# Optimization experiments

Hardware: AMD Instinct MI355X
Metric: run time of the kernel (lower is better)

The kernel has to match this reference:

```python
import jax, jax.numpy as jnp
from jax import lax
import numpy as np

B, T, H, IN = 256, 1024, 256, 1

def setup_inputs() -> dict:
    key = jax.random.key(0)
    ks = jax.random.split(key, 9)
    s = 1.0 / np.sqrt(H)  # PyTorch default uniform(-1/sqrt(H), 1/sqrt(H)); use scaled normal
    return {
        "x": jax.random.normal(ks[0], (B, T, IN), jnp.float32),
        "W_ih0": jax.random.normal(ks[1], (4 * H, IN), jnp.float32) * s,
        "W_hh0": jax.random.normal(ks[2], (4 * H, H), jnp.float32) * s,
        "b_ih0": jax.random.normal(ks[3], (4 * H,), jnp.float32) * s,
        "b_hh0": jax.random.normal(ks[4], (4 * H,), jnp.float32) * s,
        "W_ih1": jax.random.normal(ks[5], (4 * H, H), jnp.float32) * s,
        "W_hh1": jax.random.normal(ks[6], (4 * H, H), jnp.float32) * s,
        "b_ih1": jax.random.normal(ks[7], (4 * H,), jnp.float32) * s,
        "b_hh1": jax.random.normal(ks[8], (4 * H,), jnp.float32) * s,
    }

def _lstm_layer(x, W_ih, W_hh, b_ih, b_hh):
    # x: [B, T, D_in] -> (y [B, T, H], h_T [B, H], c_T [B, H]); gates ordered i,f,g,o (PyTorch)
    b, t = x.shape[0], x.shape[1]
    h = W_hh.shape[1]
    # precompute input projection for all timesteps: [T, B, 4H]
    xp = jnp.swapaxes(jnp.einsum('btd,gd->btg', x, W_ih) + b_ih + b_hh, 0, 1)

    def step(carry, xt):
        hprev, cprev = carry
        gates = xt + hprev @ W_hh.T  # [B, 4H]
        i, f, g, o = jnp.split(gates, 4, axis=-1)
        i = jax.nn.sigmoid(i)
        f = jax.nn.sigmoid(f)
        g = jnp.tanh(g)
        o = jax.nn.sigmoid(o)
        c = f * cprev + i * g
        hnew = o * jnp.tanh(c)
        return (hnew, c), hnew

    h0 = jnp.zeros((b, h), x.dtype)
    (hT, cT), ys = lax.scan(step, (h0, h0), xp)
    return jnp.swapaxes(ys, 0, 1), hT, cT

def reference(x, W_ih0, W_hh0, b_ih0, b_hh0, W_ih1, W_hh1, b_ih1, b_hh1):
    y0, h0, c0 = _lstm_layer(x, W_ih0, W_hh0, b_ih0, b_hh0)
    # inter-layer dropout(0.1) is train-only; inference = identity
    _, h1, c1 = _lstm_layer(y0, W_ih1, W_hh1, b_ih1, b_hh1)
    h_n = jnp.stack([h0, h1], axis=0)  # [num_layers, B, H]
    c_n = jnp.stack([c0, c1], axis=0)
    return h_n, c_n
```

## Files before the change

kernel.cpp:

```cpp
#include <hip/hip_runtime.h>


#define TSTEPS 1024u
#define FMAGIC 0x5A5A0000u

typedef __attribute__((ext_vector_type(8))) short bf16x8;
typedef __attribute__((ext_vector_type(4))) float f32x4;

__device__ __forceinline__ unsigned short f2bf(float f) {
  unsigned u = __float_as_uint(f);
  u += 0x7FFFu + ((u >> 16) & 1u);
  return (unsigned short)(u >> 16);
}
__device__ __forceinline__ float sigm(float x) { return 1.0f / (1.0f + __expf(-x)); }
__device__ __forceinline__ float tanh_f(float x) {
  float xc = fminf(fmaxf(x, -15.0f), 15.0f);
  float e = __expf(2.0f * xc);
  return (e - 1.0f) / (e + 1.0f);
}

__global__ __launch_bounds__(256, 1) void lstm2_v7(
    const float* __restrict__ x,
    const float* __restrict__ Wih0,
    const float* __restrict__ Whh0,
    const float* __restrict__ bih0, const float* __restrict__ bhh0,
    const float* __restrict__ Wih1,
    const float* __restrict__ Whh1,
    const float* __restrict__ bih1, const float* __restrict__ bhh1,
    float* __restrict__ out,
    unsigned long long* __restrict__ fastb,
    unsigned long long* __restrict__ slowb,
    unsigned* __restrict__ ctrl,
    unsigned* __restrict__ flagF,
    unsigned* __restrict__ flagS)
{
  const int bid  = blockIdx.x;
  const int c    = bid & 15;
  const int iw   = bid >> 4;
  const int tid  = threadIdx.x;
  const int lane = tid & 63;
  const int wv   = tid >> 6;
  const int hi   = lane >> 4;
  const int lm   = lane & 15;

  unsigned myxcc;
  asm volatile("s_getreg_b32 %0, hwreg(HW_REG_XCC_ID)" : "=s"(myxcc));
  myxcc &= 0xFu;
  if (tid == 0)
    __hip_atomic_store(&ctrl[bid], FMAGIC | myxcc,
                       __ATOMIC_RELAXED, __HIP_MEMORY_SCOPE_AGENT);

  bf16x8 w0[8], wi1[8], wh1[8];
  {
    const int wrow = (lm & 3) * 256 + (iw << 4) + (wv << 2) + (lm >> 2);
    const int kb   = hi << 3;
#pragma unroll
    for (int kk = 0; kk < 8; ++kk) {
      const int k0 = kk * 32 + kb;
      const float* p0 = Whh0 + (size_t)wrow * 256 + k0;
      const float* p1 = Wih1 + (size_t)wrow * 256 + k0;
      const float* p2 = Whh1 + (size_t)wrow * 256 + k0;
      bf16x8 a, b, cc;
#pragma unroll
      for (int e = 0; e < 8; ++e) {
        a[e]  = (short)f2bf(p0[e]);
        b[e]  = (short)f2bf(p1[e]);
        cc[e] = (short)f2bf(p2[e]);
      }
      w0[kk] = a; wi1[kk] = b; wh1[kk] = cc;
    }
  }

  const int rowE = lm;
  const int jg   = (iw << 4) + (wv << 2) + hi;
  float wx[4], bs0[4], bs1[4];
#pragma unroll
  for (int r = 0; r < 4; ++r) {
    const int col = (r << 8) + jg;
    wx[r]  = Wih0[col];
    bs0[r] = bih0[col] + bhh0[col];
    bs1[r] = bih1[col] + bhh1[col];
  }

  unsigned ofs_[8], lofs_[8];
#pragma unroll
  for (int i = 0; i < 8; ++i) {
    const int n   = tid + 256 * i;
    const int L   = n >> 10;
    const int row = (n >> 6) & 15;
    const int q   = n & 63;
    ofs_[i]  = (unsigned)(((c * 2 + L) * 16 + row) * 64 + q);
    lofs_[i] = (unsigned)(L * 4224 + row * 264 + q * 4);
  }

  __shared__ unsigned s_uni;
  if (tid == 0) {
    if (iw == 0) {
      unsigned x0 = 0, uni = 1u;
      for (int k = 0; k < 16 && uni; ++k) {
        unsigned v; int g2 = 0;
        for (;;) {
          v = __hip_atomic_load(&ctrl[c + 16 * k], __ATOMIC_RELAXED, __HIP_MEMORY_SCOPE_AGENT);
          if ((v & 0xFFFF0000u) == FMAGIC) break;
          if (++g2 > (1 << 15)) { uni = 0u; break; }
        }
        if (uni) {
          const unsigned xc = v & 0xFFFFu;
          if (k == 0) x0 = xc; else if (xc != x0) uni = 0u;
        }
      }
      __hip_atomic_store(&ctrl[256 + c], FMAGIC | uni,
                         __ATOMIC_RELAXED, __HIP_MEMORY_SCOPE_AGENT);
    }
    unsigned uni = 0u; int g2 = 0;
    for (;;) {
      unsigned v = __hip_atomic_load(&ctrl[256 + c], __ATOMIC_RELAXED, __HIP_MEMORY_SCOPE_AGENT);
      if ((v & 0xFFFF0000u) == FMAGIC) { uni = v & 1u; break; }
      if (++g2 > (1 << 15)) break;
    }
    s_uni = uni;
  }
  __syncthreads();
  const bool uniform = (s_uni != 0u);
  unsigned long long* pollD = uniform ? fastb : slowb;
  unsigned*           pollF = uniform ? flagF : flagS;
  unsigned*           myFlagF = &flagF[(c << 6) + (iw << 2) + wv];
  unsigned*           myFlagS = &flagS[(c << 6) + (iw << 2) + wv];
  unsigned*           fl      = pollF + (c << 6);

  __shared__ __align__(16) unsigned short A[2 * 2 * 16 * 264];

  const float* xrow = x + (size_t)((c << 4) + rowE) * TSTEPS;
  float4 xq = {0.f, 0.f, 0.f, 0.f};

  float c0 = 0.f, h0f = 0.f, c1 = 0.f, h1f = 0.f;
  bool dead = false;

  for (unsigned s = 0; s <= TSTEPS; ++s) {
    if ((s & 3u) == 0u && s < TSTEPS) xq = *(const float4*)(xrow + s);
    const float xv = (s & 2u) ? ((s & 1u) ? xq.w : xq.z) : ((s & 1u) ? xq.y : xq.x);

    unsigned long long* fb = fastb + (size_t)((s + 1u) & 1u) * 32768u;
    unsigned long long* sb = slowb + (size_t)((s + 1u) & 1u) * 32768u;
    const unsigned long long* pb = pollD + (size_t)(s & 1u) * 32768u;
    unsigned short* Ap = A + (s & 1u) * 8448u;

    if (s == 0) {
      for (int z = tid; z < 8448; z += 256) ((unsigned*)A)[z] = 0u;
    } else {
      const unsigned want = FMAGIC + s;
      int guard = 0;
      while (!dead) {
        const unsigned f = __hip_atomic_load(fl + lane, __ATOMIC_RELAXED, __HIP_MEMORY_SCOPE_AGENT);
        if (__all((int)((f - want) < 0x10000u))) break;
        if (++guard > (1 << 12)) dead = true;
      }
      unsigned long long vv[8];
#pragma unroll
      for (int i = 0; i < 8; ++i)
        vv[i] = __hip_atomic_load(pb + ofs_[i], __ATOMIC_RELAXED, __HIP_MEMORY_SCOPE_AGENT);
#pragma unroll
      for (int i = 0; i < 8; ++i)
        *(unsigned long long*)&Ap[lofs_[i]] = vv[i];
    }
    __syncthreads();

    bf16x8 af0[8];
    f32x4 acc0a = {0.f, 0.f, 0.f, 0.f}, acc0b = {0.f, 0.f, 0.f, 0.f};
    const unsigned short* a0p = Ap + lm * 264 + (hi << 3);
    const unsigned short* a1p = a0p + 4224;
#pragma unroll
    for (int kk = 0; kk < 4; ++kk) {
      af0[kk] = *(const bf16x8*)(a0p + kk * 32);
      acc0a = __builtin_amdgcn_mfma_f32_16x16x32_bf16(w0[kk], af0[kk], acc0a, 0, 0, 0);
    }
#pragma unroll
    for (int kk = 4; kk < 8; ++kk) {
      af0[kk] = *(const bf16x8*)(a0p + kk * 32);
      acc0b = __builtin_amdgcn_mfma_f32_16x16x32_bf16(w0[kk], af0[kk], acc0b, 0, 0, 0);
    }

    f32x4 a1a0 = {0.f, 0.f, 0.f, 0.f}, a1a1 = {0.f, 0.f, 0.f, 0.f};
    f32x4 a1b0 = {0.f, 0.f, 0.f, 0.f}, a1b1 = {0.f, 0.f, 0.f, 0.f};
#pragma unroll
    for (int kk = 0; kk < 4; ++kk) {
      a1a0 = __builtin_amdgcn_mfma_f32_16x16x32_bf16(wi1[kk], af0[kk], a1a0, 0, 0, 0);
      const bf16x8 a1f = *(const bf16x8*)(a1p + kk * 32);
      a1b0 = __builtin_amdgcn_mfma_f32_16x16x32_bf16(wh1[kk], a1f, a1b0, 0, 0, 0);
    }
#pragma unroll
    for (int kk = 4; kk < 8; ++kk) {
      a1a1 = __builtin_amdgcn_mfma_f32_16x16x32_bf16(wi1[kk], af0[kk], a1a1, 0, 0, 0);
      const bf16x8 a1f = *(const bf16x8*)(a1p + kk * 32);
      a1b1 = __builtin_amdgcn_mfma_f32_16x16x32_bf16(wh1[kk], a1f, a1b1, 0, 0, 0);
    }

    if (s < TSTEPS) {
      const float pi = (acc0a[0] + acc0b[0]) + xv * wx[0] + bs0[0];
      const float pf = (acc0a[1] + acc0b[1]) + xv * wx[1] + bs0[1];
      const float pg = (acc0a[2] + acc0b[2]) + xv * wx[2] + bs0[2];
      const float po = (acc0a[3] + acc0b[3]) + xv * wx[3] + bs0[3];
      const float ig = sigm(pi), fg = sigm(pf), gv = tanh_f(pg), og = sigm(po);
      c0  = fg * c0 + ig * gv;
      h0f = og * tanh_f(c0);

      const int v   = (int)(unsigned)f2bf(h0f);
      const int p16 = __shfl_xor(v, 16);
      const unsigned part = (unsigned)(unsigned short)v | ((unsigned)(unsigned short)p16 << 16);
      const unsigned p32  = (unsigned)__shfl_xor((int)part, 32);
      const unsigned long long v64 = (unsigned long long)part | ((unsigned long long)p32 << 32);
      const unsigned i0 = ((c * 2 + 0) * 16 + (unsigned)rowE) * 64 + (unsigned)((iw << 2) + wv);
      if (hi == 0) {
        __hip_atomic_store(fb + i0, v64, __ATOMIC_RELAXED, __HIP_MEMORY_SCOPE_WORKGROUP);
        if (!uniform)
          __hip_atomic_store(sb + i0, v64, __ATOMIC_RELAXED, __HIP_MEMORY_SCOPE_AGENT);
      }
    }

    if (s >= 1u) {
      const float pi = (a1a0[0] + a1a1[0]) + (a1b0[0] + a1b1[0]) + bs1[0];
      const float pf = (a1a0[1] + a1a1[1]) + (a1b0[1] + a1b1[1]) + bs1[1];
      const float pg = (a1a0[2] + a1a1[2]) + (a1b0[2] + a1b1[2]) + bs1[2];
      const float po = (a1a0[3] + a1a1[3]) + (a1b0[3] + a1b1[3]) + bs1[3];
      const float ig = sigm(pi), fg = sigm(pf), gv = tanh_f(pg), og = sigm(po);
      c1  = fg * c1 + ig * gv;
      h1f = og * tanh_f(c1);
    }
    if (s < TSTEPS) {
      const int v   = (int)(unsigned)f2bf(h1f);
      const int p16 = __shfl_xor(v, 16);
      const unsigned part = (unsigned)(unsigned short)v | ((unsigned)(unsigned short)p16 << 16);
      const unsigned p32  = (unsigned)__shfl_xor((int)part, 32);
      const unsigned long long v64 = (unsigned long long)part | ((unsigned long long)p32 << 32);
      const unsigned i1 = ((c * 2 + 1) * 16 + (unsigned)rowE) * 64 + (unsigned)((iw << 2) + wv);
      if (hi == 0) {
        __hip_atomic_store(fb + i1, v64, __ATOMIC_RELAXED, __HIP_MEMORY_SCOPE_WORKGROUP);
        if (!uniform)
          __hip_atomic_store(sb + i1, v64, __ATOMIC_RELAXED, __HIP_MEMORY_SCOPE_AGENT);
      }

      asm volatile("s_waitcnt vmcnt(0)" ::: "memory");
      if (lane == 0) {
        const unsigned fv = FMAGIC + s + 1u;
        if (uniform)
          __hip_atomic_store(myFlagF, fv, __ATOMIC_RELAXED, __HIP_MEMORY_SCOPE_WORKGROUP);
        else
          __hip_atomic_store(myFlagS, fv, __ATOMIC_RELAXED, __HIP_MEMORY_SCOPE_AGENT);
      }
    }
  }

  {
    const int b  = (c << 4) + rowE;
    const size_t o = (size_t)b * 256 + jg;
    out[o]                  = h0f;
    out[65536 + o]          = h1f;
    out[131072 + o]         = c0;
    out[131072 + 65536 + o] = c1;
  }
}

extern "C" void kernel_launch(void* const* d_in, const int* in_sizes, int n_in,
                              void* d_out, int out_size, void* d_ws, size_t ws_size,
                              hipStream_t stream) {
  const float* x    = (const float*)d_in[0];
  const float* Wih0 = (const float*)d_in[1];
  const float* Whh0 = (const float*)d_in[2];
  const float* bih0 = (const float*)d_in[3];
  const float* bhh0 = (const float*)d_in[4];
  const float* Wih1 = (const float*)d_in[5];
  const float* Whh1 = (const float*)d_in[6];
  const float* bih1 = (const float*)d_in[7];
  const float* bhh1 = (const float*)d_in[8];

  unsigned long long* fastb = (unsigned long long*)d_ws;
  unsigned long long* slowb;
  unsigned *ctrl, *flagF, *flagS;
  if (ws_size >= (1u << 20) + 12288u) {
    slowb = fastb + 65536;
    ctrl  = (unsigned*)(fastb + 131072);
    flagF = ctrl + 512;
    flagS = flagF + 1024;
  } else {
    slowb = fastb;
    ctrl  = (unsigned*)((char*)d_ws + (512u << 10));
    flagF = ctrl + 512;
    flagS = flagF;
  }

  lstm2_v7<<<256, 256, 0, stream>>>(x, Wih0, Whh0, bih0, bhh0,
                                    Wih1, Whh1, bih1, bhh1,
                                    (float*)d_out, fastb, slowb, ctrl, flagF, flagS);
}
```

Measured before the change: 1.807 ms.

## Split LSTM layers into separate producer/consumer blocks pipelined across timesteps

Launches twice as many blocks: one set runs layer 0 and another runs layer 1, synchronised through per-step global flags. Layer-0 blocks read their recurrent h fragments straight from global memory with no LDS staging, and they raise their wave priority. This shortens the per-step critical path of layer 0 and lets layer 1 trail it in a pipelined fashion. The cost is double the block count (launch bounds raised to 2 per CU), extra flag polling across both layers, and a write-after-read hazard on the double-buffered exchange that the extra flag checks have to cover.

```diff
diff --git a/kernel.cpp b/kernel.cpp
--- a/kernel.cpp
+++ b/kernel.cpp
@@ -19,7 +19,9 @@
   return (e - 1.0f) / (e + 1.0f);
 }
 
-__global__ __launch_bounds__(256, 1) void lstm2_v7(
+union FragU { unsigned long long q[2]; bf16x8 v; };
+
+__global__ __launch_bounds__(256, 2) void lstm2_v8(
     const float* __restrict__ x,
     const float* __restrict__ Wih0,
     const float* __restrict__ Whh0,
@@ -35,8 +37,9 @@
     unsigned* __restrict__ flagS)
 {
   const int bid  = blockIdx.x;
+  const int type = bid >> 8;
   const int c    = bid & 15;
-  const int iw   = bid >> 4;
+  const int iw   = (bid >> 4) & 15;
   const int tid  = threadIdx.x;
   const int lane = tid & 63;
   const int wv   = tid >> 6;
@@ -50,57 +53,54 @@
     __hip_atomic_store(&ctrl[bid], FMAGIC | myxcc,
                        __ATOMIC_RELAXED, __HIP_MEMORY_SCOPE_AGENT);
 
-  bf16x8 w0[8], wi1[8], wh1[8];
+  bf16x8 wA[8], wB[8];
   {
     const int wrow = (lm & 3) * 256 + (iw << 4) + (wv << 2) + (lm >> 2);
     const int kb   = hi << 3;
-#pragma unroll
-    for (int kk = 0; kk < 8; ++kk) {
-      const int k0 = kk * 32 + kb;
-      const float* p0 = Whh0 + (size_t)wrow * 256 + k0;
-      const float* p1 = Wih1 + (size_t)wrow * 256 + k0;
-      const float* p2 = Whh1 + (size_t)wrow * 256 + k0;
-      bf16x8 a, b, cc;
-#pragma unroll
-      for (int e = 0; e < 8; ++e) {
-        a[e]  = (short)f2bf(p0[e]);
-        b[e]  = (short)f2bf(p1[e]);
-        cc[e] = (short)f2bf(p2[e]);
-      }
-      w0[kk] = a; wi1[kk] = b; wh1[kk] = cc;
+    if (type == 0) {
+      const float* pA = Whh0 + (size_t)wrow * 256 + kb;
+#pragma unroll
+      for (int kk = 0; kk < 8; ++kk) {
+        bf16x8 a;
+#pragma unroll
+        for (int e = 0; e < 8; ++e) a[e] = (short)f2bf(pA[kk * 32 + e]);
+        wA[kk] = a;
+      }
+    } else {
+      const float* pA = Wih1 + (size_t)wrow * 256 + kb;
+      const float* pB = Whh1 + (size_t)wrow * 256 + kb;
+#pragma unroll
+      for (int kk = 0; kk < 8; ++kk) {
+        bf16x8 a, b;
+#pragma unroll
+        for (int e = 0; e < 8; ++e) {
+          a[e] = (short)f2bf(pA[kk * 32 + e]);
+          b[e] = (short)f2bf(pB[kk * 32 + e]);
+        }
+        wA[kk] = a; wB[kk] = b;
+      }
     }
   }
 
   const int rowE = lm;
   const int jg   = (iw << 4) + (wv << 2) + hi;
-  float wx[4], bs0[4], bs1[4];
+  float wx[4], bs[4];
 #pragma unroll
   for (int r = 0; r < 4; ++r) {
     const int col = (r << 8) + jg;
-    wx[r]  = Wih0[col];
-    bs0[r] = bih0[col] + bhh0[col];
-    bs1[r] = bih1[col] + bhh1[col];
-  }
-
-  unsigned ofs_[8], lofs_[8];
-#pragma unroll
-  for (int i = 0; i < 8; ++i) {
-    const int n   = tid + 256 * i;
-    const int L   = n >> 10;
-    const int row = (n >> 6) & 15;
-    const int q   = n & 63;
-    ofs_[i]  = (unsigned)(((c * 2 + L) * 16 + row) * 64 + q);
-    lofs_[i] = (unsigned)(L * 4224 + row * 264 + q * 4);
+    if (type == 0) { wx[r] = Wih0[col]; bs[r] = bih0[col] + bhh0[col]; }
+    else           { wx[r] = 0.f;       bs[r] = bih1[col] + bhh1[col]; }
   }
 
   __shared__ unsigned s_uni;
   if (tid == 0) {
-    if (iw == 0) {
+    if (type == 0 && iw == 0) {
       unsigned x0 = 0, uni = 1u;
-      for (int k = 0; k < 16 && uni; ++k) {
+      for (int k = 0; k < 32 && uni; ++k) {
+        const int b2 = (k < 16) ? (c + 16 * k) : (256 + c + 16 * (k - 16));
         unsigned v; int g2 = 0;
         for (;;) {
-          v = __hip_atomic_load(&ctrl[c + 16 * k], __ATOMIC_RELAXED, __HIP_MEMORY_SCOPE_AGENT);
+          v = __hip_atomic_load(&ctrl[b2], __ATOMIC_RELAXED, __HIP_MEMORY_SCOPE_AGENT);
           if ((v & 0xFFFF0000u) == FMAGIC) break;
           if (++g2 > (1 << 15)) { uni = 0u; break; }
         }
@@ -109,12 +109,12 @@
           if (k == 0) x0 = xc; else if (xc != x0) uni = 0u;
         }
       }
-      __hip_atomic_store(&ctrl[256 + c], FMAGIC | uni,
+      __hip_atomic_store(&ctrl[512 + c], FMAGIC | uni,
                          __ATOMIC_RELAXED, __HIP_MEMORY_SCOPE_AGENT);
     }
     unsigned uni = 0u; int g2 = 0;
     for (;;) {
-      unsigned v = __hip_atomic_load(&ctrl[256 + c], __ATOMIC_RELAXED, __HIP_MEMORY_SCOPE_AGENT);
+      unsigned v = __hip_atomic_load(&ctrl[512 + c], __ATOMIC_RELAXED, __HIP_MEMORY_SCOPE_AGENT);
       if ((v & 0xFFFF0000u) == FMAGIC) { uni = v & 1u; break; }
       if (++g2 > (1 << 15)) break;
     }
@@ -124,82 +124,64 @@
   const bool uniform = (s_uni != 0u);
   unsigned long long* pollD = uniform ? fastb : slowb;
   unsigned*           pollF = uniform ? flagF : flagS;
-  unsigned*           myFlagF = &flagF[(c << 6) + (iw << 2) + wv];
-  unsigned*           myFlagS = &flagS[(c << 6) + (iw << 2) + wv];
-  unsigned*           fl      = pollF + (c << 6);
-
-  __shared__ __align__(16) unsigned short A[2 * 2 * 16 * 264];
-
-  const float* xrow = x + (size_t)((c << 4) + rowE) * TSTEPS;
-  float4 xq = {0.f, 0.f, 0.f, 0.f};
-
-  float c0 = 0.f, h0f = 0.f, c1 = 0.f, h1f = 0.f;
+  unsigned*           flc   = pollF + c * 128;
+
+  const size_t oBase = (size_t)((c << 4) + rowE) * 256 + jg;
   bool dead = false;
 
-  for (unsigned s = 0; s <= TSTEPS; ++s) {
-    if ((s & 3u) == 0u && s < TSTEPS) xq = *(const float4*)(xrow + s);
-    const float xv = (s & 2u) ? ((s & 1u) ? xq.w : xq.z) : ((s & 1u) ? xq.y : xq.x);
-
-    unsigned long long* fb = fastb + (size_t)((s + 1u) & 1u) * 32768u;
-    unsigned long long* sb = slowb + (size_t)((s + 1u) & 1u) * 32768u;
-    const unsigned long long* pb = pollD + (size_t)(s & 1u) * 32768u;
-    unsigned short* Ap = A + (s & 1u) * 8448u;
-
-    if (s == 0) {
-      for (int z = tid; z < 8448; z += 256) ((unsigned*)A)[z] = 0u;
-    } else {
-      const unsigned want = FMAGIC + s;
-      int guard = 0;
-      while (!dead) {
-        const unsigned f = __hip_atomic_load(fl + lane, __ATOMIC_RELAXED, __HIP_MEMORY_SCOPE_AGENT);
-        if (__all((int)((f - want) < 0x10000u))) break;
-        if (++guard > (1 << 12)) dead = true;
-      }
-      unsigned long long vv[8];
-#pragma unroll
-      for (int i = 0; i < 8; ++i)
-        vv[i] = __hip_atomic_load(pb + ofs_[i], __ATOMIC_RELAXED, __HIP_MEMORY_SCOPE_AGENT);
-#pragma unroll
-      for (int i = 0; i < 8; ++i)
-        *(unsigned long long*)&Ap[lofs_[i]] = vv[i];
-    }
-    __syncthreads();
-
-    bf16x8 af0[8];
-    f32x4 acc0a = {0.f, 0.f, 0.f, 0.f}, acc0b = {0.f, 0.f, 0.f, 0.f};
-    const unsigned short* a0p = Ap + lm * 264 + (hi << 3);
-    const unsigned short* a1p = a0p + 4224;
-#pragma unroll
-    for (int kk = 0; kk < 4; ++kk) {
-      af0[kk] = *(const bf16x8*)(a0p + kk * 32);
-      acc0a = __builtin_amdgcn_mfma_f32_16x16x32_bf16(w0[kk], af0[kk], acc0a, 0, 0, 0);
-    }
-#pragma unroll
-    for (int kk = 4; kk < 8; ++kk) {
-      af0[kk] = *(const bf16x8*)(a0p + kk * 32);
-      acc0b = __builtin_amdgcn_mfma_f32_16x16x32_bf16(w0[kk], af0[kk], acc0b, 0, 0, 0);
-    }
-
-    f32x4 a1a0 = {0.f, 0.f, 0.f, 0.f}, a1a1 = {0.f, 0.f, 0.f, 0.f};
-    f32x4 a1b0 = {0.f, 0.f, 0.f, 0.f}, a1b1 = {0.f, 0.f, 0.f, 0.f};
-#pragma unroll
-    for (int kk = 0; kk < 4; ++kk) {
-      a1a0 = __builtin_amdgcn_mfma_f32_16x16x32_bf16(wi1[kk], af0[kk], a1a0, 0, 0, 0);
-      const bf16x8 a1f = *(const bf16x8*)(a1p + kk * 32);
-      a1b0 = __builtin_amdgcn_mfma_f32_16x16x32_bf16(wh1[kk], a1f, a1b0, 0, 0, 0);
-    }
-#pragma unroll
-    for (int kk = 4; kk < 8; ++kk) {
-      a1a1 = __builtin_amdgcn_mfma_f32_16x16x32_bf16(wi1[kk], af0[kk], a1a1, 0, 0, 0);
-      const bf16x8 a1f = *(const bf16x8*)(a1p + kk * 32);
-      a1b1 = __builtin_amdgcn_mfma_f32_16x16x32_bf16(wh1[kk], a1f, a1b1, 0, 0, 0);
-    }
-
-    if (s < TSTEPS) {
-      const float pi = (acc0a[0] + acc0b[0]) + xv * wx[0] + bs0[0];
-      const float pf = (acc0a[1] + acc0b[1]) + xv * wx[1] + bs0[1];
-      const float pg = (acc0a[2] + acc0b[2]) + xv * wx[2] + bs0[2];
-      const float po = (acc0a[3] + acc0b[3]) + xv * wx[3] + bs0[3];
+  if (type == 0) {
+    __builtin_amdgcn_s_setprio(1);
+    unsigned* myF = &flagF[c * 128 + (iw << 2) + wv];
+    unsigned* myS = &flagS[c * 128 + (iw << 2) + wv];
+    const float* xrow = x + (size_t)((c << 4) + rowE) * TSTEPS;
+    float4 xq = {0.f, 0.f, 0.f, 0.f};
+    float c0 = 0.f, h0f = 0.f;
+
+    for (unsigned s = 0; s < TSTEPS; ++s) {
+      if ((s & 3u) == 0u) xq = *(const float4*)(xrow + s);
+      const float xv = (s & 2u) ? ((s & 1u) ? xq.w : xq.z) : ((s & 1u) ? xq.y : xq.x);
+
+      bf16x8 af0[8];
+      if (s == 0) {
+        const bf16x8 z = {0, 0, 0, 0, 0, 0, 0, 0};
+#pragma unroll
+        for (int kk = 0; kk < 8; ++kk) af0[kk] = z;
+      } else {
+        const unsigned want0 = FMAGIC + s;
+        const unsigned want1 = FMAGIC + s - 1u;
+        const bool chk1 = (s >= 2u);
+        int guard = 0;
+        while (!dead) {
+          const unsigned f0 = __hip_atomic_load(flc + lane, __ATOMIC_RELAXED, __HIP_MEMORY_SCOPE_AGENT);
+          const unsigned f1 = chk1 ? __hip_atomic_load(flc + 64 + lane, __ATOMIC_RELAXED, __HIP_MEMORY_SCOPE_AGENT)
+                                   : want1;
+          const bool ok = ((f0 - want0) < 0x10000u) & ((f1 - want1) < 0x10000u);
+          if (__all(ok)) break;
+          if (++guard > (1 << 13)) dead = true;
+        }
+        const unsigned long long* hb =
+            pollD + (size_t)(s & 1u) * 32768u + (c << 11) + (lm << 6) + (hi << 1);
+#pragma unroll
+        for (int kk = 0; kk < 8; ++kk) {
+          FragU u;
+          u.q[0] = __hip_atomic_load(hb + kk * 8,     __ATOMIC_RELAXED, __HIP_MEMORY_SCOPE_AGENT);
+          u.q[1] = __hip_atomic_load(hb + kk * 8 + 1, __ATOMIC_RELAXED, __HIP_MEMORY_SCOPE_AGENT);
+          af0[kk] = u.v;
+        }
+      }
+
+      f32x4 aca = {0.f, 0.f, 0.f, 0.f}, acb = {0.f, 0.f, 0.f, 0.f};
+#pragma unroll
+      for (int kk = 0; kk < 4; ++kk)
+        aca = __builtin_amdgcn_mfma_f32_16x16x32_bf16(wA[kk], af0[kk], aca, 0, 0, 0);
+#pragma unroll
+      for (int kk = 4; kk < 8; ++kk)
+        acb = __builtin_amdgcn_mfma_f32_16x16x32_bf16(wA[kk], af0[kk], acb, 0, 0, 0);
+
+      const float pi = (aca[0] + acb[0]) + xv * wx[0] + bs[0];
+      const float pf = (aca[1] + acb[1]) + xv * wx[1] + bs[1];
+      const float pg = (aca[2] + acb[2]) + xv * wx[2] + bs[2];
+      const float po = (aca[3] + acb[3]) + xv * wx[3] + bs[3];
       const float ig = sigm(pi), fg = sigm(pf), gv = tanh_f(pg), og = sigm(po);
       c0  = fg * c0 + ig * gv;
       h0f = og * tanh_f(c0);
@@ -210,53 +192,133 @@
       const unsigned p32  = (unsigned)__shfl_xor((int)part, 32);
       const unsigned long long v64 = (unsigned long long)part | ((unsigned long long)p32 << 32);
       const unsigned i0 = ((c * 2 + 0) * 16 + (unsigned)rowE) * 64 + (unsigned)((iw << 2) + wv);
+      unsigned long long* fb = fastb + (size_t)((s + 1u) & 1u) * 32768u;
+      unsigned long long* sb = slowb + (size_t)((s + 1u) & 1u) * 32768u;
       if (hi == 0) {
         __hip_atomic_store(fb + i0, v64, __ATOMIC_RELAXED, __HIP_MEMORY_SCOPE_WORKGROUP);
         if (!uniform)
           __hip_atomic_store(sb + i0, v64, __ATOMIC_RELAXED, __HIP_MEMORY_SCOPE_AGENT);
       }
-    }
-
-    if (s >= 1u) {
-      const float pi = (a1a0[0] + a1a1[0]) + (a1b0[0] + a1b1[0]) + bs1[0];
-      const float pf = (a1a0[1] + a1a1[1]) + (a1b0[1] + a1b1[1]) + bs1[1];
-      const float pg = (a1a0[2] + a1a1[2]) + (a1b0[2] + a1b1[2]) + bs1[2];
-      const float po = (a1a0[3] + a1a1[3]) + (a1b0[3] + a1b1[3]) + bs1[3];
+      asm volatile("s_waitcnt vmcnt(0)" ::: "memory");
+      if (lane == 0) {
+        const unsigned fv = FMAGIC + s + 1u;
+        if (uniform)
+          __hip_atomic_store(myF, fv, __ATOMIC_RELAXED, __HIP_MEMORY_SCOPE_WORKGROUP);
+        else
+          __hip_atomic_store(myS, fv, __ATOMIC_RELAXED, __HIP_MEMORY_SCOPE_AGENT);
+      }
+    }
+    out[oBase]          = h0f;
+    out[131072 + oBase] = c0;
+
+  } else {
+    unsigned* myF = &flagF[c * 128 + 64 + (iw << 2) + wv];
+    unsigned* myS = &flagS[c * 128 + 64 + (iw << 2) + wv];
+
+    unsigned ofs_[8], lofs_[8];
+#pragma unroll
+    for (int i = 0; i < 8; ++i) {
+      const int n   = tid + 256 * i;
+      const int L   = n >> 10;
+      const int row = (n >> 6) & 15;
+      const int q   = n & 63;
+      ofs_[i]  = (unsigned)(((c * 2 + L) * 16 + row) * 64 + q);
+      lofs_[i] = (unsigned)(L * 4224 + row * 264 + q * 4);
+    }
+
+    __shared__ __align__(16) unsigned short A[2 * 2 * 16 * 264];
+    for (int z = tid; z < 8448; z += 256) ((unsigned*)A)[z] = 0u;
+    __syncthreads();
+
+    float c1 = 0.f, h1f = 0.f;
+
+    for (unsigned t = 0; t < TSTEPS; ++t) {
+      {
+        const unsigned want0 = FMAGIC + t + 1u;
+        const unsigned want1 = FMAGIC + t;
+        const bool chk1 = (t >= 1u);
+        int guard = 0;
+        while (!dead) {
+          const unsigned f0 = __hip_atomic_load(flc + lane, __ATOMIC_RELAXED, __HIP_MEMORY_SCOPE_AGENT);
+          const unsigned f1 = chk1 ? __hip_atomic_load(flc + 64 + lane, __ATOMIC_RELAXED, __HIP_MEMORY_SCOPE_AGENT)
+                                   : want1;
+          const bool ok = ((f0 - want0) < 0x10000u) & ((f1 - want1) < 0x10000u);
+          if (__all(ok)) break;
+          if (++guard > (1 << 13)) { dead = true; break; }
+          __builtin_amdgcn_s_sleep(1);
+        }
+      }
+      const unsigned long long* pb0 = pollD + (size_t)((t + 1u) & 1u) * 32768u;
+      const unsigned long long* pb1 = pollD + (size_t)(t & 1u) * 32768u;
+      unsigned short* Ap = A + (t & 1u) * 8448u;
+      {
+        unsigned long long vv[8];
+#pragma unroll
+        for (int i = 0; i < 4; ++i)
+          vv[i] = __hip_atomic_load(pb0 + ofs_[i], __ATOMIC_RELAXED, __HIP_MEMORY_SCOPE_AGENT);
+        if (t >= 1u) {
+#pragma unroll
+          for (int i = 4; i < 8; ++i)
+            vv[i] = __hip_atomic_load(pb1 + ofs_[i], __ATOMIC_RELAXED, __HIP_MEMORY_SCOPE_AGENT);
+        }
+#pragma unroll
+        for (int i = 0; i < 4; ++i)
+          *(unsigned long long*)&Ap[lofs_[i]] = vv[i];
+        if (t >= 1u) {
+#pragma unroll
+          for (int i = 4; i < 8; ++i)
+            *(unsigned long long*)&Ap[lofs_[i]] = vv[i];
+        }
+      }
+      __syncthreads();
+
+      const unsigned short* a0p = Ap + lm * 264 + (hi << 3);
+      const unsigned short* a1p = a0p + 4224;
+      f32x4 p0 = {0.f,0.f,0.f,0.f}, p1 = {0.f,0.f,0.f,0.f};
+      f32x4 q0 = {0.f,0.f,0.f,0.f}, q1 = {0.f,0.f,0.f,0.f};
+#pragma unroll
+      for (int kk = 0; kk < 4; ++kk) {
+        p0 = __builtin_amdgcn_mfma_f32_16x16x32_bf16(wA[kk], *(const bf16x8*)(a0p + kk * 32), p0, 0, 0, 0);
+        q0 = __builtin_amdgcn_mfma_f32_16x16x32_bf16(wB[kk], *(const bf16x8*)(a1p + kk * 32), q0, 0, 0, 0);
+      }
+#pragma unroll
+      for (int kk = 4; kk < 8; ++kk) {
+        p1 = __builtin_amdgcn_mfma_f32_16x16x32_bf16(wA[kk], *(const bf16x8*)(a0p + kk * 32), p1, 0, 0, 0);
+        q1 = __builtin_amdgcn_mfma_f32_16x16x32_bf16(wB[kk], *(const bf16x8*)(a1p + kk * 32), q1, 0, 0, 0);
+      }
+
+      const float pi = (p0[0] + p1[0]) + (q0[0] + q1[0]) + bs[0];
+      const float pf = (p0[1] + p1[1]) + (q0[1] + q1[1]) + bs[1];
+      const float pg = (p0[2] + p1[2]) + (q0[2] + q1[2]) + bs[2];
+      const float po = (p0[3] + p1[3]) + (q0[3] + q1[3]) + bs[3];
       const float ig = sigm(pi), fg = sigm(pf), gv = tanh_f(pg), og = sigm(po);
       c1  = fg * c1 + ig * gv;
       h1f = og * tanh_f(c1);
-    }
-    if (s < TSTEPS) {
+
       const int v   = (int)(unsigned)f2bf(h1f);
       const int p16 = __shfl_xor(v, 16);
       const unsigned part = (unsigned)(unsigned short)v | ((unsigned)(unsigned short)p16 << 16);
       const unsigned p32  = (unsigned)__shfl_xor((int)part, 32);
       const unsigned long long v64 = (unsigned long long)part | ((unsigned long long)p32 << 32);
       const unsigned i1 = ((c * 2 + 1) * 16 + (unsigned)rowE) * 64 + (unsigned)((iw << 2) + wv);
+      unsigned long long* fb = fastb + (size_t)((t + 1u) & 1u) * 32768u;
+      unsigned long long* sb = slowb + (size_t)((t + 1u) & 1u) * 32768u;
       if (hi == 0) {
         __hip_atomic_store(fb + i1, v64, __ATOMIC_RELAXED, __HIP_MEMORY_SCOPE_WORKGROUP);
         if (!uniform)
           __hip_atomic_store(sb + i1, v64, __ATOMIC_RELAXED, __HIP_MEMORY_SCOPE_AGENT);
       }
-
       asm volatile("s_waitcnt vmcnt(0)" ::: "memory");
       if (lane == 0) {
-        const unsigned fv = FMAGIC + s + 1u;
+        const unsigned fv = FMAGIC + t + 1u;
         if (uniform)
-          __hip_atomic_store(myFlagF, fv, __ATOMIC_RELAXED, __HIP_MEMORY_SCOPE_WORKGROUP);
+          __hip_atomic_store(myF, fv, __ATOMIC_RELAXED, __HIP_MEMORY_SCOPE_WORKGROUP);
         else
-          __hip_atomic_store(myFlagS, fv, __ATOMIC_RELAXED, __HIP_MEMORY_SCOPE_AGENT);
-      }
-    }
-  }
-
-  {
-    const int b  = (c << 4) + rowE;
-    const size_t o = (size_t)b * 256 + jg;
-    out[o]                  = h0f;
-    out[65536 + o]          = h1f;
-    out[131072 + o]         = c0;
-    out[131072 + 65536 + o] = c1;
+          __hip_atomic_store(myS, fv, __ATOMIC_RELAXED, __HIP_MEMORY_SCOPE_AGENT);
+      }
+    }
+    out[65536 + oBase]          = h1f;
+    out[131072 + 65536 + oBase] = c1;
   }
 }
 
@@ -276,19 +338,19 @@
   unsigned long long* fastb = (unsigned long long*)d_ws;
   unsigned long long* slowb;
   unsigned *ctrl, *flagF, *flagS;
-  if (ws_size >= (1u << 20) + 12288u) {
+  if (ws_size >= (1u << 20) + 24576u) {
     slowb = fastb + 65536;
     ctrl  = (unsigned*)(fastb + 131072);
-    flagF = ctrl + 512;
-    flagS = flagF + 1024;
+    flagF = ctrl + 2048;
+    flagS = flagF + 2048;
   } else {
     slowb = fastb;
     ctrl  = (unsigned*)((char*)d_ws + (512u << 10));
-    flagF = ctrl + 512;
+    flagF = ctrl + 2048;
     flagS = flagF;
   }
 
-  lstm2_v7<<<256, 256, 0, stream>>>(x, Wih0, Whh0, bih0, bhh0,
+  lstm2_v8<<<512, 256, 0, stream>>>(x, Wih0, Whh0, bih0, bhh0,
                                     Wih1, Whh1, bih1, bhh1,
                                     (float*)d_out, fastb, slowb, ctrl, flagF, flagS);
 }
```

After: 3.335 ms. 1.85x slower.

## Split per-layer flags, stage x in LDS, and publish layer-0 state earlier

Applied to the files above, without the earlier changes.

Layer-0 hidden state is now computed and published, with its own flag, right after its MFMA chain and before the layer-1 MFMAs run. Other blocks can therefore start their next step sooner instead of waiting for both layers. The input sequence x is preloaded into padded shared memory, replacing per-step global float4 loads. Stores are narrowed to 32-bit with a different packing, and the layer-0 MFMA chain is split across four accumulators to shorten the dependency chain. In exchange, pollers must check twice as many flags, and the extra flag write and vmcnt wait per step add overhead.

```diff
diff --git a/kernel.cpp b/kernel.cpp
--- a/kernel.cpp
+++ b/kernel.cpp
@@ -19,7 +19,7 @@
   return (e - 1.0f) / (e + 1.0f);
 }
 
-__global__ __launch_bounds__(256, 1) void lstm2_v7(
+__global__ __launch_bounds__(256, 1) void lstm2_v9(
     const float* __restrict__ x,
     const float* __restrict__ Wih0,
     const float* __restrict__ Whh0,
@@ -71,8 +71,7 @@
     }
   }
 
-  const int rowE = lm;
-  const int jg   = (iw << 4) + (wv << 2) + hi;
+  const int jg = (iw << 4) + (wv << 2) + hi;
   float wx[4], bs0[4], bs1[4];
 #pragma unroll
   for (int r = 0; r < 4; ++r) {
@@ -80,6 +79,15 @@
     wx[r]  = Wih0[col];
     bs0[r] = bih0[col] + bhh0[col];
     bs1[r] = bih1[col] + bhh1[col];
+  }
+
+  __shared__ __align__(16) unsigned short A[2 * 2 * 16 * 264];
+  __shared__ float XL[16 * 1041];
+
+  {
+    const float* xsrc = x + (size_t)(c << 4) * TSTEPS;
+    for (int idx = tid; idx < 16 * 1024; idx += 256)
+      XL[(idx >> 10) * 1041 + (idx & 1023)] = xsrc[idx];
   }
 
   unsigned ofs_[8], lofs_[8];
@@ -124,26 +132,20 @@
   const bool uniform = (s_uni != 0u);
   unsigned long long* pollD = uniform ? fastb : slowb;
   unsigned*           pollF = uniform ? flagF : flagS;
-  unsigned*           myFlagF = &flagF[(c << 6) + (iw << 2) + wv];
-  unsigned*           myFlagS = &flagS[(c << 6) + (iw << 2) + wv];
-  unsigned*           fl      = pollF + (c << 6);
-
-  __shared__ __align__(16) unsigned short A[2 * 2 * 16 * 264];
-
-  const float* xrow = x + (size_t)((c << 4) + rowE) * TSTEPS;
-  float4 xq = {0.f, 0.f, 0.f, 0.f};
+  unsigned*           fl    = pollF + c * 128;
+  unsigned*           myF0F = &flagF[c * 128 + (iw << 2) + wv];
+  unsigned*           myF0S = &flagS[c * 128 + (iw << 2) + wv];
+  unsigned*           myF1F = myF0F + 64;
+  unsigned*           myF1S = myF0S + 64;
 
   float c0 = 0.f, h0f = 0.f, c1 = 0.f, h1f = 0.f;
   bool dead = false;
 
   for (unsigned s = 0; s <= TSTEPS; ++s) {
-    if ((s & 3u) == 0u && s < TSTEPS) xq = *(const float4*)(xrow + s);
-    const float xv = (s & 2u) ? ((s & 1u) ? xq.w : xq.z) : ((s & 1u) ? xq.y : xq.x);
-
-    unsigned long long* fb = fastb + (size_t)((s + 1u) & 1u) * 32768u;
-    unsigned long long* sb = slowb + (size_t)((s + 1u) & 1u) * 32768u;
     const unsigned long long* pb = pollD + (size_t)(s & 1u) * 32768u;
     unsigned short* Ap = A + (s & 1u) * 8448u;
+    unsigned* fb32 = (unsigned*)(fastb + (size_t)((s + 1u) & 1u) * 32768u);
+    unsigned* sb32 = (unsigned*)(slowb + (size_t)((s + 1u) & 1u) * 32768u);
 
     if (s == 0) {
       for (int z = tid; z < 8448; z += 256) ((unsigned*)A)[z] = 0u;
@@ -151,9 +153,10 @@
       const unsigned want = FMAGIC + s;
       int guard = 0;
       while (!dead) {
-        const unsigned f = __hip_atomic_load(fl + lane, __ATOMIC_RELAXED, __HIP_MEMORY_SCOPE_AGENT);
-        if (__all((int)((f - want) < 0x10000u))) break;
-        if (++guard > (1 << 12)) dead = true;
+        const unsigned f0 = __hip_atomic_load(fl + lane,      __ATOMIC_RELAXED, __HIP_MEMORY_SCOPE_AGENT);
+        const unsigned f1 = __hip_atomic_load(fl + 64 + lane, __ATOMIC_RELAXED, __HIP_MEMORY_SCOPE_AGENT);
+        if (__all(((f0 - want) < 0x10000u) & ((f1 - want) < 0x10000u))) break;
+        if (++guard > (1 << 14)) dead = true;
       }
       unsigned long long vv[8];
 #pragma unroll
@@ -166,92 +169,101 @@
     __syncthreads();
 
     bf16x8 af0[8];
-    f32x4 acc0a = {0.f, 0.f, 0.f, 0.f}, acc0b = {0.f, 0.f, 0.f, 0.f};
     const unsigned short* a0p = Ap + lm * 264 + (hi << 3);
     const unsigned short* a1p = a0p + 4224;
-#pragma unroll
-    for (int kk = 0; kk < 4; ++kk) {
-      af0[kk] = *(const bf16x8*)(a0p + kk * 32);
-      acc0a = __builtin_amdgcn_mfma_f32_16x16x32_bf16(w0[kk], af0[kk], acc0a, 0, 0, 0);
-    }
-#pragma unroll
-    for (int kk = 4; kk < 8; ++kk) {
-      af0[kk] = *(const bf16x8*)(a0p + kk * 32);
-      acc0b = __builtin_amdgcn_mfma_f32_16x16x32_bf16(w0[kk], af0[kk], acc0b, 0, 0, 0);
-    }
-
-    f32x4 a1a0 = {0.f, 0.f, 0.f, 0.f}, a1a1 = {0.f, 0.f, 0.f, 0.f};
-    f32x4 a1b0 = {0.f, 0.f, 0.f, 0.f}, a1b1 = {0.f, 0.f, 0.f, 0.f};
-#pragma unroll
-    for (int kk = 0; kk < 4; ++kk) {
-      a1a0 = __builtin_amdgcn_mfma_f32_16x16x32_bf16(wi1[kk], af0[kk], a1a0, 0, 0, 0);
-      const bf16x8 a1f = *(const bf16x8*)(a1p + kk * 32);
-      a1b0 = __builtin_amdgcn_mfma_f32_16x16x32_bf16(wh1[kk], a1f, a1b0, 0, 0, 0);
-    }
-#pragma unroll
-    for (int kk = 4; kk < 8; ++kk) {
-      a1a1 = __builtin_amdgcn_mfma_f32_16x16x32_bf16(wi1[kk], af0[kk], a1a1, 0, 0, 0);
-      const bf16x8 a1f = *(const bf16x8*)(a1p + kk * 32);
-      a1b1 = __builtin_amdgcn_mfma_f32_16x16x32_bf16(wh1[kk], a1f, a1b1, 0, 0, 0);
-    }
-
+    f32x4 A0 = {0.f,0.f,0.f,0.f}, A1 = {0.f,0.f,0.f,0.f};
+    f32x4 A2 = {0.f,0.f,0.f,0.f}, A3 = {0.f,0.f,0.f,0.f};
+#pragma unroll
+    for (int kk = 0; kk < 8; ++kk) af0[kk] = *(const bf16x8*)(a0p + kk * 32);
+    A0 = __builtin_amdgcn_mfma_f32_16x16x32_bf16(w0[0], af0[0], A0, 0, 0, 0);
+    A1 = __builtin_amdgcn_mfma_f32_16x16x32_bf16(w0[1], af0[1], A1, 0, 0, 0);
+    A2 = __builtin_amdgcn_mfma_f32_16x16x32_bf16(w0[2], af0[2], A2, 0, 0, 0);
+    A3 = __builtin_amdgcn_mfma_f32_16x16x32_bf16(w0[3], af0[3], A3, 0, 0, 0);
+    A0 = __builtin_amdgcn_mfma_f32_16x16x32_bf16(w0[4], af0[4], A0, 0, 0, 0);
+    A1 = __builtin_amdgcn_mfma_f32_16x16x32_bf16(w0[5], af0[5], A1, 0, 0, 0);
+    A2 = __builtin_amdgcn_mfma_f32_16x16x32_bf16(w0[6], af0[6], A2, 0, 0, 0);
+    A3 = __builtin_amdgcn_mfma_f32_16x16x32_bf16(w0[7], af0[7], A3, 0, 0, 0);
+
+    const float xv = XL[lm * 1041 + (int)(s < TSTEPS ? s : 0u)];
     if (s < TSTEPS) {
-      const float pi = (acc0a[0] + acc0b[0]) + xv * wx[0] + bs0[0];
-      const float pf = (acc0a[1] + acc0b[1]) + xv * wx[1] + bs0[1];
-      const float pg = (acc0a[2] + acc0b[2]) + xv * wx[2] + bs0[2];
-      const float po = (acc0a[3] + acc0b[3]) + xv * wx[3] + bs0[3];
+      const float pi = (A0[0] + A1[0]) + (A2[0] + A3[0]) + xv * wx[0] + bs0[0];
+      const float pf = (A0[1] + A1[1]) + (A2[1] + A3[1]) + xv * wx[1] + bs0[1];
+      const float pg = (A0[2] + A1[2]) + (A2[2] + A3[2]) + xv * wx[2] + bs0[2];
+      const float po = (A0[3] + A1[3]) + (A2[3] + A3[3]) + xv * wx[3] + bs0[3];
       const float ig = sigm(pi), fg = sigm(pf), gv = tanh_f(pg), og = sigm(po);
       c0  = fg * c0 + ig * gv;
       h0f = og * tanh_f(c0);
 
       const int v   = (int)(unsigned)f2bf(h0f);
       const int p16 = __shfl_xor(v, 16);
-      const unsigned part = (unsigned)(unsigned short)v | ((unsigned)(unsigned short)p16 << 16);
-      const unsigned p32  = (unsigned)__shfl_xor((int)part, 32);
-      const unsigned long long v64 = (unsigned long long)part | ((unsigned long long)p32 << 32);
-      const unsigned i0 = ((c * 2 + 0) * 16 + (unsigned)rowE) * 64 + (unsigned)((iw << 2) + wv);
-      if (hi == 0) {
-        __hip_atomic_store(fb + i0, v64, __ATOMIC_RELAXED, __HIP_MEMORY_SCOPE_WORKGROUP);
+      if ((hi & 1) == 0) {
+        const unsigned val = (unsigned)(unsigned short)v |
+                             ((unsigned)(unsigned short)p16 << 16);
+        const unsigned idx = (unsigned)(((c * 2 + 0) * 16 + lm) * 128 +
+                                        (iw << 3) + (wv << 1) + (hi >> 1));
+        __hip_atomic_store(fb32 + idx, val, __ATOMIC_RELAXED, __HIP_MEMORY_SCOPE_WORKGROUP);
         if (!uniform)
-          __hip_atomic_store(sb + i0, v64, __ATOMIC_RELAXED, __HIP_MEMORY_SCOPE_AGENT);
-      }
-    }
-
-    if (s >= 1u) {
-      const float pi = (a1a0[0] + a1a1[0]) + (a1b0[0] + a1b1[0]) + bs1[0];
-      const float pf = (a1a0[1] + a1a1[1]) + (a1b0[1] + a1b1[1]) + bs1[1];
-      const float pg = (a1a0[2] + a1a1[2]) + (a1b0[2] + a1b1[2]) + bs1[2];
-      const float po = (a1a0[3] + a1a1[3]) + (a1b0[3] + a1b1[3]) + bs1[3];
-      const float ig = sigm(pi), fg = sigm(pf), gv = tanh_f(pg), og = sigm(po);
-      c1  = fg * c1 + ig * gv;
-      h1f = og * tanh_f(c1);
-    }
-    if (s < TSTEPS) {
-      const int v   = (int)(unsigned)f2bf(h1f);
-      const int p16 = __shfl_xor(v, 16);
-      const unsigned part = (unsigned)(unsigned short)v | ((unsigned)(unsigned short)p16 << 16);
-      const unsigned p32  = (unsigned)__shfl_xor((int)part, 32);
-      const unsigned long long v64 = (unsigned long long)part | ((unsigned long long)p32 << 32);
-      const unsigned i1 = ((c * 2 + 1) * 16 + (unsigned)rowE) * 64 + (unsigned)((iw << 2) + wv);
-      if (hi == 0) {
-        __hip_atomic_store(fb + i1, v64, __ATOMIC_RELAXED, __HIP_MEMORY_SCOPE_WORKGROUP);
-        if (!uniform)
-          __hip_atomic_store(sb + i1, v64, __ATOMIC_RELAXED, __HIP_MEMORY_SCOPE_AGENT);
-      }
-
+          __hip_atomic_store(sb32 + idx, val, __ATOMIC_RELAXED, __HIP_MEMORY_SCOPE_AGENT);
+      }
       asm volatile("s_waitcnt vmcnt(0)" ::: "memory");
       if (lane == 0) {
         const unsigned fv = FMAGIC + s + 1u;
         if (uniform)
-          __hip_atomic_store(myFlagF, fv, __ATOMIC_RELAXED, __HIP_MEMORY_SCOPE_WORKGROUP);
+          __hip_atomic_store(myF0F, fv, __ATOMIC_RELAXED, __HIP_MEMORY_SCOPE_WORKGROUP);
         else
-          __hip_atomic_store(myFlagS, fv, __ATOMIC_RELAXED, __HIP_MEMORY_SCOPE_AGENT);
+          __hip_atomic_store(myF0S, fv, __ATOMIC_RELAXED, __HIP_MEMORY_SCOPE_AGENT);
+      }
+    }
+
+    f32x4 B0 = {0.f,0.f,0.f,0.f}, B1 = {0.f,0.f,0.f,0.f};
+    f32x4 B2 = {0.f,0.f,0.f,0.f}, B3 = {0.f,0.f,0.f,0.f};
+#pragma unroll
+    for (int kk = 0; kk < 4; ++kk) {
+      B0 = __builtin_amdgcn_mfma_f32_16x16x32_bf16(wi1[kk], af0[kk], B0, 0, 0, 0);
+      const bf16x8 a1f = *(const bf16x8*)(a1p + kk * 32);
+      B1 = __builtin_amdgcn_mfma_f32_16x16x32_bf16(wh1[kk], a1f, B1, 0, 0, 0);
+    }
+#pragma unroll
+    for (int kk = 4; kk < 8; ++kk) {
+      B2 = __builtin_amdgcn_mfma_f32_16x16x32_bf16(wi1[kk], af0[kk], B2, 0, 0, 0);
+      const bf16x8 a1f = *(const bf16x8*)(a1p + kk * 32);
+      B3 = __builtin_amdgcn_mfma_f32_16x16x32_bf16(wh1[kk], a1f, B3, 0, 0, 0);
+    }
+
+    if (s >= 1u) {
+      const float pi = (B0[0] + B1[0]) + (B2[0] + B3[0]) + bs1[0];
+      const float pf = (B0[1] + B1[1]) + (B2[1] + B3[1]) + bs1[1];
+      const float pg = (B0[2] + B1[2]) + (B2[2] + B3[2]) + bs1[2];
+      const float po = (B0[3] + B1[3]) + (B2[3] + B3[3]) + bs1[3];
+      const float ig = sigm(pi), fg = sigm(pf), gv = tanh_f(pg), og = sigm(po);
+      c1  = fg * c1 + ig * gv;
+      h1f = og * tanh_f(c1);
+    }
+    if (s < TSTEPS) {
+      const int v   = (int)(unsigned)f2bf(h1f);
+      const int p16 = __shfl_xor(v, 16);
+      if ((hi & 1) == 0) {
+        const unsigned val = (unsigned)(unsigned short)v |
+                             ((unsigned)(unsigned short)p16 << 16);
+        const unsigned idx = (unsigned)(((c * 2 + 1) * 16 + lm) * 128 +
+                                        (iw << 3) + (wv << 1) + (hi >> 1));
+        __hip_atomic_store(fb32 + idx, val, __ATOMIC_RELAXED, __HIP_MEMORY_SCOPE_WORKGROUP);
+        if (!uniform)
+          __hip_atomic_store(sb32 + idx, val, __ATOMIC_RELAXED, __HIP_MEMORY_SCOPE_AGENT);
+      }
+      asm volatile("s_waitcnt vmcnt(0)" ::: "memory");
+      if (lane == 0) {
+        const unsigned fv = FMAGIC + s + 1u;
+        if (uniform)
+          __hip_atomic_store(myF1F, fv, __ATOMIC_RELAXED, __HIP_MEMORY_SCOPE_WORKGROUP);
+        else
+          __hip_atomic_store(myF1S, fv, __ATOMIC_RELAXED, __HIP_MEMORY_SCOPE_AGENT);
       }
     }
   }
 
   {
-    const int b  = (c << 4) + rowE;
+    const int b  = (c << 4) + lm;
     const size_t o = (size_t)b * 256 + jg;
     out[o]                  = h0f;
     out[65536 + o]          = h1f;
@@ -276,19 +288,19 @@
   unsigned long long* fastb = (unsigned long long*)d_ws;
   unsigned long long* slowb;
   unsigned *ctrl, *flagF, *flagS;
-  if (ws_size >= (1u << 20) + 12288u) {
+  if (ws_size >= (1u << 20) + 24576u) {
     slowb = fastb + 65536;
     ctrl  = (unsigned*)(fastb + 131072);
-    flagF = ctrl + 512;
-    flagS = flagF + 1024;
+    flagF = ctrl + 2048;
+    flagS = flagF + 2048;
   } else {
     slowb = fastb;
     ctrl  = (unsigned*)((char*)d_ws + (512u << 10));
-    flagF = ctrl + 512;
+    flagF = ctrl + 2048;
     flagS = flagF;
   }
 
-  lstm2_v7<<<256, 256, 0, stream>>>(x, Wih0, Whh0, bih0, bhh0,
+  lstm2_v9<<<256, 256, 0, stream>>>(x, Wih0, Whh0, bih0, bhh0,
                                     Wih1, Whh1, bih1, bhh1,
                                     (float*)d_out, fastb, slowb, ctrl, flagF, flagS);
 }
```

Result: slower. 1.878 ms (+4.0%).
